# Kernel tuning notes

Hardware: AMD Instinct MI355X
Metric: run time of the kernel (lower is better)

Reference implementation:

```python
import jax, jax.numpy as jnp
import numpy as np

L = 4          # num transformer layers
C = 128        # embed_dim
P = 16         # patch size
NH = 8         # num heads
HD = C // NH   # head dim
SCALE = HD ** -0.5
THRESH = [0.001, 0.0012, 0.0015, 0.002]
EPS = 1e-5


def _ln(x, w, b):
    mu = jnp.mean(x, -1, keepdims=True)
    v = jnp.mean(jnp.square(x - mu), -1, keepdims=True)
    return (x - mu) * jax.lax.rsqrt(v + EPS) * w + b


def _attn(x, qw, qb, ow, ob):
    B, N, _ = x.shape
    qkv = (x @ qw + qb).reshape(B, N, 3, NH, HD)
    q, k, v = jnp.moveaxis(qkv, 2, 0)                      # each [B,N,NH,HD]
    q = q.transpose(0, 2, 1, 3)
    k = k.transpose(0, 2, 1, 3)
    v = v.transpose(0, 2, 1, 3)                            # [B,NH,N,HD]
    probs = jax.nn.softmax(jnp.einsum('bhnd,bhmd->bhnm', q, k) * SCALE, axis=-1)
    o = jnp.einsum('bhnm,bhmd->bhnd', probs, v).transpose(0, 2, 1, 3).reshape(B, N, C)
    return o @ ow + ob, probs


def _layer(x, i, ln1_w, ln1_b, qkv_w, qkv_b, out_w, out_b, ln2_w, ln2_b, w1, b1, w2, b2):
    a, probs = _attn(_ln(x, ln1_w[i], ln1_b[i]), qkv_w[i], qkv_b[i], out_w[i], out_b[i])
    x = x + a
    h = jax.nn.gelu(_ln(x, ln2_w[i], ln2_b[i]) @ w1[i] + b1[i], approximate=False)
    return x + h @ w2[i] + b2[i], probs


def forward(conv_w, conv_b, cls_token, pos_embed, ln1_w, ln1_b, qkv_w, qkv_b,
            out_w, out_b, ln2_w, ln2_b, mlp_w1, mlp_b1, mlp_w2, mlp_b2, x, meta=None):
    B = x.shape[0]
    Hh, Ww = x.shape[2] // P, x.shape[3] // P
    # patch embed == conv with kernel=stride=P, expressed as a patch matmul
    xr = x.reshape(B, 3, Hh, P, Ww, P).transpose(0, 2, 4, 1, 3, 5).reshape(B, Hh * Ww, 3 * P * P)
    tok = xr @ conv_w.reshape(C, -1).T + conv_b           # [B, nH*nW, C]
    x = jnp.concatenate([jnp.broadcast_to(cls_token, (B, 1, C)), tok], axis=1) + pos_embed
    meta_out = []
    for i in range(L):
        x, probs = _layer(x, i, ln1_w, ln1_b, qkv_w, qkv_b, out_w, out_b,
                          ln2_w, ln2_b, mlp_w1, mlp_b1, mlp_w2, mlp_b2)
        if i < L - 1:
            cls_t, tokens = x[:, :1], x[:, 1:]
            if meta is None:
                am = jnp.mean(probs[:, :, 1:, 0], axis=1)  # [B, N] attn of tokens to cls
                keep = am > THRESH[i]
                fb = keep.sum(1) == 0                      # fallback: keep argmax token
                keep = keep | (fb[:, None] & (jnp.arange(am.shape[1])[None, :] == jnp.argmax(am, 1)[:, None]))
                count = keep.sum(1)
                order = jnp.argsort(~keep, axis=1)         # stable: kept tokens first, in order
                mk = int(jnp.max(count))
                order, count = np.asarray(order), np.asarray(count)
                meta_out.append((order, count, mk))
            else:
                order, count, mk = meta[i]
            g = jnp.take_along_axis(tokens, jnp.asarray(order[:, :mk])[:, :, None], axis=1)
            valid = (jnp.arange(mk)[None, :] < jnp.asarray(count)[:, None]).astype(tokens.dtype)
            x = jnp.concatenate([cls_t, g * valid[:, :, None]], axis=1)
            # original re-adds pos_embed[0:1+mk] regardless of which tokens survived
            x = x + jnp.concatenate([pos_embed[:, :1], pos_embed[:, 1:1 + mk]], axis=1)
    return x, meta_out


def setup_inputs() -> dict:
    key = jax.random.key(0)
    ks = jax.random.split(key, 8)
    def w(k, shape, fan_in):
        return jax.random.normal(k, shape, jnp.float32) / np.float32(np.sqrt(fan_in))
    N_POS = (512 // P) * (512 // P) + 1  # 1025
    return {
        'conv_w': w(ks[0], (C, 3, P, P), 3 * P * P),
        'conv_b': jnp.zeros((C,), jnp.float32),
        'cls_token': jnp.zeros((1, 1, C), jnp.float32),
        'pos_embed': 0.02 * jax.random.truncated_normal(ks[1], -2.0, 2.0, (1, N_POS, C), jnp.float32),
        'ln1_w': jnp.ones((L, C), jnp.float32), 'ln1_b': jnp.zeros((L, C), jnp.float32),
        'qkv_w': w(ks[2], (L, C, 3 * C), C), 'qkv_b': jnp.zeros((L, 3 * C), jnp.float32),
        'out_w': w(ks[3], (L, C, C), C), 'out_b': jnp.zeros((L, C), jnp.float32),
        'ln2_w': jnp.ones((L, C), jnp.float32), 'ln2_b': jnp.zeros((L, C), jnp.float32),
        'mlp_w1': w(ks[4], (L, C, 4 * C), C), 'mlp_b1': jnp.zeros((L, 4 * C), jnp.float32),
        'mlp_w2': w(ks[5], (L, 4 * C, C), 4 * C), 'mlp_b2': jnp.zeros((L, C), jnp.float32),
        'x': jax.random.normal(ks[6], (8, 3, 512, 512), jnp.float32),
    }


def reference(conv_w, conv_b, cls_token, pos_embed, ln1_w, ln1_b, qkv_w, qkv_b,
              out_w, out_b, ln2_w, ln2_b, mlp_w1, mlp_b1, mlp_w2, mlp_b2, x):
    out, _ = forward(conv_w, conv_b, cls_token, pos_embed, ln1_w, ln1_b, qkv_w, qkv_b,
                     out_w, out_b, ln2_w, ln2_b, mlp_w1, mlp_b1, mlp_w2, mlp_b2, x)
    return out
```

## Files before the change

### kernel.cpp

```cpp
#include <hip/hip_runtime.h>
#include <hip/hip_bf16.h>
#include <math.h>

typedef __hip_bfloat16 bf16;
typedef __attribute__((ext_vector_type(4))) _Float16 half4;
typedef __attribute__((ext_vector_type(4))) float f32x4;

#define NMAX 1025
#define TMAX 1024
#define BATCH 8
#define CH 128
#define NHEAD 8
#define HDIM 16
#define MMAX (BATCH * NMAX)
#define QGRID 17
#define VSTRIDE 1028
#define POSZ 1049600
#define KCHUNK 192

__device__ __forceinline__ float b2f(bf16 v) { return __bfloat162float(v); }

__device__ __forceinline__ bool is_bf16(const void* ln1w_raw) {
    return ((const unsigned*)ln1w_raw)[0] == 0x3F803F80u;
}
__device__ __forceinline__ float ldsel(const void* p, size_t i, bool bf) {
    return bf ? __bfloat162float(((const bf16*)p)[i]) : ((const float*)p)[i];
}

struct CvtDesc { const void* src; float* dst; int cnt; };
struct CvtPack { CvtDesc d[15]; };

__global__ void convert_kernel(CvtPack p, const void* ln1w_raw, int* nTok) {
    bool bf = is_bf16(ln1w_raw);
    CvtDesc dd = p.d[blockIdx.y];
    int idx = blockIdx.x * 256 + threadIdx.x;
    if (idx < dd.cnt) dd.dst[idx] = ldsel(dd.src, idx, bf);
    if (blockIdx.y == 0 && idx == 0) nTok[0] = NMAX;
}

__global__ void prep_kernel(const void* conv_w, float* __restrict__ wT,
                            const void* ln1w_raw) {
    bool bf = is_bf16(ln1w_raw);
    int idx = blockIdx.x * 256 + threadIdx.x;
    if (idx < 768 * 128) {
        int k = idx >> 7, oc = idx & 127;
        wT[idx] = ldsel(conv_w, (size_t)oc * 768 + k, bf);
    }
}

__global__ __launch_bounds__(128) void patch_partial(
        const void* __restrict__ img, const float* __restrict__ wT,
        float* __restrict__ partial, const void* ln1w_raw) {
    __shared__ float pbuf[8 * KCHUNK];
    bool bf = is_bf16(ln1w_raw);
    int b = blockIdx.y;
    int g = blockIdx.x & 127;
    int kc = blockIdx.x >> 7;
    int tid = threadIdx.x;
    int t0 = g * 8;
    int kbase = kc * KCHUNK;
    const int NV = 8 * KCHUNK / 4;
    for (int i = tid; i < NV; i += 128) {
        int e = i << 2;
        int t = e / KCHUNK, kloc = e - t * KCHUNK;
        int k = kbase + kloc;
        int c = k >> 8, rem = k & 255, p1 = rem >> 4, p2 = rem & 15;
        int hw = t0 + t;
        int h = hw >> 5, w = hw & 31;
        size_t a = (((size_t)(b * 3 + c) * 512) + h * 16 + p1) * 512 + w * 16 + p2;
        float4 v;
        if (bf) {
            ushort4 u = *(const ushort4*)((const unsigned short*)img + a);
            v.x = __uint_as_float((unsigned)u.x << 16);
            v.y = __uint_as_float((unsigned)u.y << 16);
            v.z = __uint_as_float((unsigned)u.z << 16);
            v.w = __uint_as_float((unsigned)u.w << 16);
        } else {
            v = *(const float4*)((const float*)img + a);
        }
        *(float4*)&pbuf[e] = v;
    }
    __syncthreads();
    float acc[8];
#pragma unroll
    for (int t = 0; t < 8; t++) acc[t] = 0.f;
    const float* wc = wT + (size_t)kbase * 128;
    for (int k4 = 0; k4 < KCHUNK; k4 += 4) {
        float w0 = wc[(k4 + 0) * 128 + tid];
        float w1 = wc[(k4 + 1) * 128 + tid];
        float w2 = wc[(k4 + 2) * 128 + tid];
        float w3 = wc[(k4 + 3) * 128 + tid];
#pragma unroll
        for (int t = 0; t < 8; t++) {
            const float4 a = *(const float4*)&pbuf[t * KCHUNK + k4];
            acc[t] = fmaf(a.x, w0, acc[t]);
            acc[t] = fmaf(a.y, w1, acc[t]);
            acc[t] = fmaf(a.z, w2, acc[t]);
            acc[t] = fmaf(a.w, w3, acc[t]);
        }
    }
    float* pp = partial + ((size_t)(kc * 8 + b) * 1024 + t0) * 128 + tid;
#pragma unroll
    for (int t = 0; t < 8; t++) pp[(size_t)t * 128] = acc[t];
}

__global__ __launch_bounds__(256) void patch_reduce(
        const float* __restrict__ partial, const float* __restrict__ conv_b,
        const float* __restrict__ cls_tok, const float* __restrict__ pos,
        float* __restrict__ out) {
    if (blockIdx.x == 4096) {
        for (int i = threadIdx.x; i < 8 * 128; i += 256) {
            int b = i >> 7, c = i & 127;
            out[(size_t)(b * NMAX) * CH + c] = cls_tok[c] + pos[c];
        }
        return;
    }
    int idx = blockIdx.x * 256 + threadIdx.x;
    int tg = idx >> 7;
    int col = idx & 127;
    int b = tg >> 10, tok = tg & 1023;
    size_t pi = ((size_t)b * 1024 + tok) * 128 + col;
    const size_t PSTRIDE = (size_t)8 * 1024 * 128;
    float v = partial[pi] + partial[pi + PSTRIDE]
            + partial[pi + 2 * PSTRIDE] + partial[pi + 3 * PSTRIDE];
    out[((size_t)(b * NMAX) + 1 + tok) * CH + col] =
        v + conv_b[col] + pos[(size_t)(1 + tok) * CH + col];
}

template <int K, int NCOL, int CTILE, int ROWS, bool LN, bool GELU_ACT,
          bool RESID, bool QKV_SPLIT>
__global__ void mm_kernel(const float* __restrict__ A, const float* __restrict__ W,
                          const float* __restrict__ bias, const float* __restrict__ lnw,
                          const float* __restrict__ lnb, const float* __restrict__ R,
                          float* __restrict__ out, _Float16* __restrict__ kout,
                          _Float16* __restrict__ vout, const int* __restrict__ nPtr) {
    __shared__ float As[ROWS * K];
    int N = nPtr[0];
    int M = BATCH * N;
    int row0 = blockIdx.x * ROWS;
    if (row0 >= M) return;
    int tid = threadIdx.x;
    for (int i = tid; i < ROWS * K / 4; i += CTILE) {
        int e = i << 2;
        int r = e / K, rem = e % K;
        float4 v;
        int row = row0 + r;
        if (row < M)
            v = *(const float4*)&A[(size_t)row * K + rem];
        else
            v = make_float4(0.f, 0.f, 0.f, 0.f);
        *(float4*)&As[r * K + rem] = v;
    }
    __syncthreads();
    if (LN) {
        int wid = tid >> 6, lane = tid & 63;
        const int NW = CTILE / 64;
        float wl0 = lnw[lane], wl1 = lnw[64 + lane];
        float bl0 = lnb[lane], bl1 = lnb[64 + lane];
        for (int r = wid; r < ROWS; r += NW) {
            float x0 = As[r * K + lane], x1 = As[r * K + 64 + lane];
            float s = x0 + x1;
#pragma unroll
            for (int off = 32; off; off >>= 1) s += __shfl_xor(s, off);
            float mu = s * (1.f / 128.f);
            float d0 = x0 - mu, d1 = x1 - mu;
            float v = d0 * d0 + d1 * d1;
#pragma unroll
            for (int off = 32; off; off >>= 1) v += __shfl_xor(v, off);
            float inv = 1.f / sqrtf(v * (1.f / 128.f) + 1e-5f);
            As[r * K + lane] = d0 * inv * wl0 + bl0;
            As[r * K + 64 + lane] = d1 * inv * wl1 + bl1;
        }
        __syncthreads();
    }
    float acc[ROWS];
#pragma unroll
    for (int r = 0; r < ROWS; r++) acc[r] = 0.f;
    int col = tid;
    for (int k4 = 0; k4 < K; k4 += 4) {
        float w0 = W[(size_t)(k4 + 0) * NCOL + col];
        float w1 = W[(size_t)(k4 + 1) * NCOL + col];
        float w2 = W[(size_t)(k4 + 2) * NCOL + col];
        float w3 = W[(size_t)(k4 + 3) * NCOL + col];
#pragma unroll
        for (int r = 0; r < ROWS; r++) {
            const float4 a = *(const float4*)&As[r * K + k4];
            acc[r] = fmaf(a.x, w0, acc[r]);
            acc[r] = fmaf(a.y, w1, acc[r]);
            acc[r] = fmaf(a.z, w2, acc[r]);
            acc[r] = fmaf(a.w, w3, acc[r]);
        }
    }
    float bv = bias[col];
    int rmax = min(ROWS, M - row0);
    if (QKV_SPLIT) {
        int part = col >> 7;
        int c128 = col & 127;
        int hh = c128 >> 4, dd = c128 & 15;
        for (int r = 0; r < rmax; r++) {
            float v = acc[r] + bv;
            int row = row0 + r;
            if (part == 0) {
                out[(size_t)row * 128 + c128] = v;
            } else {
                int bb = row / N, nn = row - (row / N) * N;
                if (part == 1) {
                    _Float16 hi = (_Float16)v;
                    _Float16 lo = (_Float16)(v - (float)hi);
                    size_t kb2 = ((size_t)(bb * 8 + hh) * NMAX + nn) * 32 + dd;
                    kout[kb2] = hi;
                    kout[kb2 + 16] = lo;
                } else {
                    vout[((size_t)(bb * 8 + hh) * 16 + dd) * VSTRIDE + nn] = (_Float16)v;
                }
            }
        }
        if (blockIdx.x == 0 && part == 2) {
            int zn = min(16, VSTRIDE - N);
            for (int bb = 0; bb < 8; bb++) {
                size_t rb = ((size_t)((bb * 8 + hh) * 16 + dd)) * VSTRIDE;
                for (int i = 0; i < zn; i++) vout[rb + N + i] = (_Float16)0.f;
            }
            if (hh == 7 && dd == 15) {
                for (int i = 0; i < 16; i++)
                    vout[(size_t)1024 * VSTRIDE + i] = (_Float16)0.f;
            }
        }
    } else {
        for (int r = 0; r < rmax; r++) {
            float v = acc[r] + bv;
            if (GELU_ACT) v = 0.5f * v * (1.f + erff(v * 0.70710678118654752f));
            if (RESID) v += R[(size_t)(row0 + r) * NCOL + col];
            out[(size_t)(row0 + r) * NCOL + col] = v;
        }
    }
}

__global__ __launch_bounds__(256) void attn_kernel(
        const float* __restrict__ qbuf, const _Float16* __restrict__ kbuf,
        const _Float16* __restrict__ vbuf, float* __restrict__ oout,
        float* __restrict__ clsp, const int* __restrict__ nPtr) {
    int N = nPtr[0];
    int bid = blockIdx.x;
    int b = bid & 7;
    int h = (bid >> 3) & 7;
    int qg = bid >> 6;
    int wave = threadIdx.x >> 6;
    int lane = threadIdx.x & 63;
    int qt = qg * 4 + wave;
    if (qt * 16 >= N) return;
    int ql = lane & 15;
    int hig = lane >> 4;
    int nq = qt * 16 + ql;
    int nqc = min(nq, N - 1);
    half4 qhi, qlo;
    {
        const float4 qv = *(const float4*)(qbuf + ((size_t)(b * N + nqc)) * 128 + h * HDIM + hig * 4);
        float q0 = qv.x * 0.25f, q1 = qv.y * 0.25f, q2 = qv.z * 0.25f, q3 = qv.w * 0.25f;
        qhi[0] = (_Float16)q0; qlo[0] = (_Float16)(q0 - (float)qhi[0]);
        qhi[1] = (_Float16)q1; qlo[1] = (_Float16)(q1 - (float)qhi[1]);
        qhi[2] = (_Float16)q2; qlo[2] = (_Float16)(q2 - (float)qhi[2]);
        qhi[3] = (_Float16)q3; qlo[3] = (_Float16)(q3 - (float)qhi[3]);
    }
    const _Float16* kb = kbuf + (size_t)(b * 8 + h) * NMAX * 32;
    const _Float16* vt = vbuf + ((size_t)(b * 8 + h) * 16 + ql) * VSTRIDE;
    f32x4 of = {0.f, 0.f, 0.f, 0.f};
    const f32x4 zz = {0.f, 0.f, 0.f, 0.f};
    float m = -3.0e38f, l = 0.f, s0raw = 0.f;
    int ntFull = N >> 4;
    int t = 0;
    for (; t + 2 <= ntFull; t += 2) {
        int k0 = t * 16;
        const _Float16* kpA = kb + ((size_t)(k0 + ql)) * 32 + hig * 4;
        const _Float16* kpB = kpA + 16 * 32;
        half4 khiA = *(const half4*)(kpA);
        half4 kloA = *(const half4*)(kpA + 16);
        half4 khiB = *(const half4*)(kpB);
        half4 kloB = *(const half4*)(kpB + 16);
        f32x4 sA1 = __builtin_amdgcn_mfma_f32_16x16x16f16(khiA, qhi, zz, 0, 0, 0);
        f32x4 sB1 = __builtin_amdgcn_mfma_f32_16x16x16f16(khiB, qhi, zz, 0, 0, 0);
        f32x4 sA2 = __builtin_amdgcn_mfma_f32_16x16x16f16(khiA, qlo, zz, 0, 0, 0);
        f32x4 sB2 = __builtin_amdgcn_mfma_f32_16x16x16f16(khiB, qlo, zz, 0, 0, 0);
        sA2 = __builtin_amdgcn_mfma_f32_16x16x16f16(kloA, qhi, sA2, 0, 0, 0);
        sB2 = __builtin_amdgcn_mfma_f32_16x16x16f16(kloB, qhi, sB2, 0, 0, 0);
        f32x4 saA = sA1 + sA2;
        f32x4 saB = sB1 + sB2;
        if (t == 0) s0raw = saA[0];
        float mcA = fmaxf(fmaxf(saA[0], saA[1]), fmaxf(saA[2], saA[3]));
        float mcB = fmaxf(fmaxf(saB[0], saB[1]), fmaxf(saB[2], saB[3]));
        float mc = fmaxf(mcA, mcB);
        mc = fmaxf(mc, __shfl_xor(mc, 16));
        mc = fmaxf(mc, __shfl_xor(mc, 32));
        if (!__all(mc <= m)) {
            float mnew = fmaxf(m, mc);
            float corr = __expf(m - mnew);
            l *= corr;
#pragma unroll
            for (int r = 0; r < 4; r++)
                of[r] *= __shfl(corr, hig * 4 + r);
            m = mnew;
        }
        float pA0 = __expf(saA[0] - m), pA1 = __expf(saA[1] - m);
        float pA2 = __expf(saA[2] - m), pA3 = __expf(saA[3] - m);
        float pB0 = __expf(saB[0] - m), pB1 = __expf(saB[1] - m);
        float pB2 = __expf(saB[2] - m), pB3 = __expf(saB[3] - m);
        l += ((pA0 + pA1) + (pA2 + pA3)) + ((pB0 + pB1) + (pB2 + pB3));
        half4 pfA, pfB;
        pfA[0] = (_Float16)pA0; pfA[1] = (_Float16)pA1;
        pfA[2] = (_Float16)pA2; pfA[3] = (_Float16)pA3;
        pfB[0] = (_Float16)pB0; pfB[1] = (_Float16)pB1;
        pfB[2] = (_Float16)pB2; pfB[3] = (_Float16)pB3;
        half4 vfA = *(const half4*)(vt + k0 + hig * 4);
        half4 vfB = *(const half4*)(vt + k0 + 16 + hig * 4);
        of = __builtin_amdgcn_mfma_f32_16x16x16f16(pfA, vfA, of, 0, 0, 0);
        of = __builtin_amdgcn_mfma_f32_16x16x16f16(pfB, vfB, of, 0, 0, 0);
    }
    if (t < ntFull) {
        int k0 = t * 16;
        const _Float16* kp = kb + ((size_t)(k0 + ql)) * 32 + hig * 4;
        half4 khi = *(const half4*)(kp);
        half4 klo = *(const half4*)(kp + 16);
        f32x4 s1 = __builtin_amdgcn_mfma_f32_16x16x16f16(khi, qhi, zz, 0, 0, 0);
        f32x4 s2 = __builtin_amdgcn_mfma_f32_16x16x16f16(khi, qlo, zz, 0, 0, 0);
        s2 = __builtin_amdgcn_mfma_f32_16x16x16f16(klo, qhi, s2, 0, 0, 0);
        f32x4 sa = s1 + s2;
        if (t == 0) s0raw = sa[0];
        float mc = fmaxf(fmaxf(sa[0], sa[1]), fmaxf(sa[2], sa[3]));
        mc = fmaxf(mc, __shfl_xor(mc, 16));
        mc = fmaxf(mc, __shfl_xor(mc, 32));
        if (!__all(mc <= m)) {
            float mnew = fmaxf(m, mc);
            float corr = __expf(m - mnew);
            l *= corr;
#pragma unroll
            for (int r = 0; r < 4; r++)
                of[r] *= __shfl(corr, hig * 4 + r);
            m = mnew;
        }
        float p0 = __expf(sa[0] - m), p1 = __expf(sa[1] - m);
        float p2 = __expf(sa[2] - m), p3 = __expf(sa[3] - m);
        l += (p0 + p1) + (p2 + p3);
        half4 pf;
        pf[0] = (_Float16)p0; pf[1] = (_Float16)p1;
        pf[2] = (_Float16)p2; pf[3] = (_Float16)p3;
        half4 vf = *(const half4*)(vt + k0 + hig * 4);
        of = __builtin_amdgcn_mfma_f32_16x16x16f16(pf, vf, of, 0, 0, 0);
        t++;
    }
    int k0t = ntFull * 16;
    if (k0t < N) {
        int kk = min(k0t + ql, N - 1);
        const _Float16* kp = kb + (size_t)kk * 32 + hig * 4;
        half4 khi = *(const half4*)(kp);
        half4 klo = *(const half4*)(kp + 16);
        f32x4 s1 = __builtin_amdgcn_mfma_f32_16x16x16f16(khi, qhi, zz, 0, 0, 0);
        f32x4 s2 = __builtin_amdgcn_mfma_f32_16x16x16f16(khi, qlo, zz, 0, 0, 0);
        s2 = __builtin_amdgcn_mfma_f32_16x16x16f16(klo, qhi, s2, 0, 0, 0);
        f32x4 sa = s1 + s2;
        if (ntFull == 0) s0raw = sa[0];
        float s0 = (k0t + hig * 4 + 0 < N) ? sa[0] : -3.0e38f;
        float s1m = (k0t + hig * 4 + 1 < N) ? sa[1] : -3.0e38f;
        float s2m = (k0t + hig * 4 + 2 < N) ? sa[2] : -3.0e38f;
        float s3m = (k0t + hig * 4 + 3 < N) ? sa[3] : -3.0e38f;
        float mc = fmaxf(fmaxf(s0, s1m), fmaxf(s2m, s3m));
        mc = fmaxf(mc, __shfl_xor(mc, 16));
        mc = fmaxf(mc, __shfl_xor(mc, 32));
        if (!__all(mc <= m)) {
            float mnew = fmaxf(m, mc);
            float corr = __expf(m - mnew);
            l *= corr;
#pragma unroll
            for (int r = 0; r < 4; r++)
                of[r] *= __shfl(corr, hig * 4 + r);
            m = mnew;
        }
        float p0 = __expf(s0 - m);
        float p1 = __expf(s1m - m);
        float p2 = __expf(s2m - m);
        float p3 = __expf(s3m - m);
        l += (p0 + p1) + (p2 + p3);
        half4 pf;
        pf[0] = (_Float16)p0; pf[1] = (_Float16)p1;
        pf[2] = (_Float16)p2; pf[3] = (_Float16)p3;
        half4 vf = *(const half4*)(vt + k0t + hig * 4);
        of = __builtin_amdgcn_mfma_f32_16x16x16f16(pf, vf, of, 0, 0, 0);
    }
    l += __shfl_xor(l, 16);
    l += __shfl_xor(l, 32);
    float linv = 1.f / l;
#pragma unroll
    for (int r = 0; r < 4; r++) {
        int qq = qt * 16 + hig * 4 + r;
        if (qq < N) {
            float ov = of[r] * __shfl(linv, hig * 4 + r);
            oout[((size_t)(b * N + qq)) * 128 + h * HDIM + ql] = ov;
        }
    }
    if (hig == 0 && nq >= 1 && nq < N) {
        clsp[(size_t)(b * 8 + h) * TMAX + (nq - 1)] = __expf(s0raw - m) * linv;
    }
}

__global__ __launch_bounds__(1024) void prune_kernel(const float* __restrict__ clsp,
                                                     int* __restrict__ order,
                                                     int* __restrict__ cnt,
                                                     const int* __restrict__ nPtr, int layer) {
    __shared__ int sdata[1024];
    __shared__ float wv_[16];
    __shared__ int wi_[16];
    __shared__ int wc_[16];
    __shared__ int sArg, sCnt0;
    int b = blockIdx.x;
    int t = threadIdx.x;
    int N = nPtr[0];
    int T = N - 1;
    float am = -1.f;
    if (t < T) {
        float s = 0.f;
#pragma unroll
        for (int h = 0; h < 8; h++) s += clsp[((size_t)(b * 8 + h)) * TMAX + t];
        am = s * 0.125f;
    }
    const double TH[4] = {0.001, 0.0012, 0.0015, 0.002};
    int keep = (t < T) && ((double)am > TH[layer]);
    float bv = am;
    int bi = t;
    int kc = keep;
#pragma unroll
    for (int off = 32; off; off >>= 1) {
        float ov = __shfl_xor(bv, off);
        int oi = __shfl_xor(bi, off);
        if (ov > bv || (ov == bv && oi < bi)) { bv = ov; bi = oi; }
        kc += __shfl_xor(kc, off);
    }
    int wid = t >> 6, lane = t & 63;
    if (lane == 0) { wv_[wid] = bv; wi_[wid] = bi; wc_[wid] = kc; }
    __syncthreads();
    if (t == 0) {
        float Bv = wv_[0];
        int Bi = wi_[0], C = 0;
        for (int w = 0; w < 16; w++) {
            C += wc_[w];
            if (wv_[w] > Bv || (wv_[w] == Bv && wi_[w] < Bi)) { Bv = wv_[w]; Bi = wi_[w]; }
        }
        sArg = Bi;
        sCnt0 = C;
    }
    __syncthreads();
    if (sCnt0 == 0) keep = (t == sArg) && (t < T);
    sdata[t] = keep;
    __syncthreads();
    for (int off = 1; off < 1024; off <<= 1) {
        int v = sdata[t];
        int add = (t >= off) ? sdata[t - off] : 0;
        __syncthreads();
        sdata[t] = v + add;
        __syncthreads();
    }
    int incl = sdata[t];
    int total = sdata[1023];
    if (t < T) {
        if (keep)
            order[b * TMAX + (incl - 1)] = t;
        else
            order[b * TMAX + total + t - incl] = t;
    }
    if (t == 0) cnt[b] = total;
}

__global__ __launch_bounds__(256) void gather_kernel(
        const float* __restrict__ xin, float* __restrict__ xout,
        const int* __restrict__ order, const int* __restrict__ cnt,
        const float* __restrict__ pos, const int* __restrict__ nPtr,
        int* __restrict__ nNext) {
    int Nold = nPtr[0];
    int mk = cnt[0];
#pragma unroll
    for (int i = 1; i < 8; i++) mk = max(mk, cnt[i]);
    int Nnew = mk + 1;
    if (blockIdx.x == 0 && blockIdx.y == 0 && threadIdx.x == 0) nNext[0] = Nnew;
    int b = blockIdx.y;
    int j = blockIdx.x * 2 + (threadIdx.x >> 7);
    int c = threadIdx.x & 127;
    if (j >= Nnew) return;
    float v;
    if (j == 0)
        v = xin[((size_t)(b * Nold)) * CH + c];
    else {
        int src = order[b * TMAX + (j - 1)];
        v = (j - 1 < cnt[b]) ? xin[((size_t)(b * Nold + 1 + src)) * CH + c] : 0.f;
    }
    xout[((size_t)(b * Nnew + j)) * CH + c] = v + pos[(size_t)j * CH + c];
}

__global__ void outconv_kernel(const float* __restrict__ xin, void* __restrict__ out,
                               int total, const void* ln1w_raw) {
    bool bf = is_bf16(ln1w_raw);
    int i = blockIdx.x * 256 + threadIdx.x;
    if (i < total) {
        if (bf) ((bf16*)out)[i] = __float2bfloat16(xin[i]);
        else    ((float*)out)[i] = xin[i];
    }
}

extern "C" void kernel_launch(void* const* d_in, const int* in_sizes, int n_in,
                              void* d_out, int out_size, void* d_ws, size_t ws_size,
                              hipStream_t stream) {
    const void* conv_w = d_in[0];
    const void* conv_b = d_in[1];
    const void* cls_token = d_in[2];
    const void* pos_embed = d_in[3];
    const void* ln1_w = d_in[4];
    const void* ln1_b = d_in[5];
    const void* qkv_w = d_in[6];
    const void* qkv_b = d_in[7];
    const void* out_w = d_in[8];
    const void* out_b = d_in[9];
    const void* ln2_w = d_in[10];
    const void* ln2_b = d_in[11];
    const void* mlp_w1 = d_in[12];
    const void* mlp_b1 = d_in[13];
    const void* mlp_w2 = d_in[14];
    const void* mlp_b2 = d_in[15];
    const void* img = d_in[16];

    float* ws = (float*)d_ws;
    size_t off = 0;
    float* bufA = ws + off; off += POSZ;
    float* bufB = ws + off; off += POSZ;
    float* obuf = ws + off; off += POSZ;
    float* tmp  = ws + off; off += (size_t)BATCH * NMAX * 512;
    float* wT   = ws + off; off += 768 * 128;
    float* clsp = ws + off; off += (size_t)BATCH * NHEAD * TMAX;
    int* order  = (int*)(ws + off); off += BATCH * TMAX;
    int* cnt    = (int*)(ws + off); off += 16;
    int* nTok   = (int*)(ws + off); off += 16;
    float* wts  = ws + off;
    const size_t wts_total = 924544;

    float* qbuf = tmp;
    _Float16* kbuf = (_Float16*)(tmp + POSZ);
    _Float16* vbuf = (_Float16*)(tmp + 2 * POSZ);

    float* f_conv_b = wts + 0;
    float* f_cls    = wts + 128;
    float* f_pos    = wts + 256;
    float* f_ln1w   = wts + 131456;
    float* f_ln1b   = wts + 131968;
    float* f_qkvw   = wts + 132480;
    float* f_qkvb   = wts + 329088;
    float* f_outw   = wts + 330624;
    float* f_outb   = wts + 396160;
    float* f_ln2w   = wts + 396672;
    float* f_ln2b   = wts + 397184;
    float* f_w1     = wts + 397696;
    float* f_b1     = wts + 659840;
    float* f_w2     = wts + 661888;
    float* f_b2     = wts + 924032;

    CvtPack pk;
    pk.d[0]  = {conv_b,    f_conv_b, 128};
    pk.d[1]  = {cls_token, f_cls,    128};
    pk.d[2]  = {pos_embed, f_pos,    131200};
    pk.d[3]  = {ln1_w,     f_ln1w,   512};
    pk.d[4]  = {ln1_b,     f_ln1b,   512};
    pk.d[5]  = {qkv_w,     f_qkvw,   196608};
    pk.d[6]  = {qkv_b,     f_qkvb,   1536};
    pk.d[7]  = {out_w,     f_outw,   65536};
    pk.d[8]  = {out_b,     f_outb,   512};
    pk.d[9]  = {ln2_w,     f_ln2w,   512};
    pk.d[10] = {ln2_b,     f_ln2b,   512};
    pk.d[11] = {mlp_w1,    f_w1,     262144};
    pk.d[12] = {mlp_b1,    f_b1,     2048};
    pk.d[13] = {mlp_w2,    f_w2,     262144};
    pk.d[14] = {mlp_b2,    f_b2,     512};

    convert_kernel<<<dim3(1024, 15), 256, 0, stream>>>(pk, ln1_w, nTok);
    prep_kernel<<<(768 * 128 + 255) / 256, 256, 0, stream>>>(conv_w, wT, ln1_w);
    patch_partial<<<dim3(512, BATCH), 128, 0, stream>>>(img, wT, tmp, ln1_w);
    patch_reduce<<<4097, 256, 0, stream>>>(tmp, f_conv_b, f_cls, f_pos, bufA);

    float* xc = bufA;
    float* xalt = bufB;
    const int GR8 = (MMAX + 7) / 8;

    for (int i = 0; i < 4; i++) {
        const int* nP = nTok + i;
        mm_kernel<128, 384, 384, 8, true, false, false, true>
            <<<GR8, 384, 0, stream>>>(
            xc, f_qkvw + (size_t)i * 128 * 384, f_qkvb + i * 384,
            f_ln1w + i * 128, f_ln1b + i * 128, nullptr, qbuf, kbuf, vbuf, nP);
        attn_kernel<<<QGRID * 64, 256, 0, stream>>>(
            qbuf, kbuf, vbuf, qbuf, clsp, nP);
        mm_kernel<128, 128, 128, 8, false, false, true, false>
            <<<GR8, 128, 0, stream>>>(
            qbuf, f_outw + (size_t)i * 128 * 128, f_outb + i * 128,
            nullptr, nullptr, xc, xalt, nullptr, nullptr, nP);
        mm_kernel<128, 512, 512, 8, true, true, false, false>
            <<<GR8, 512, 0, stream>>>(
            xalt, f_w1 + (size_t)i * 128 * 512, f_b1 + i * 512,
            f_ln2w + i * 128, f_ln2b + i * 128, nullptr, tmp, nullptr, nullptr, nP);
        mm_kernel<512, 128, 128, 8, false, false, true, false>
            <<<GR8, 128, 0, stream>>>(
            tmp, f_w2 + (size_t)i * 512 * 128, f_b2 + i * 128,
            nullptr, nullptr, xalt, xc, nullptr, nullptr, nP);
        if (i < 3) {
            prune_kernel<<<BATCH, 1024, 0, stream>>>(clsp, order, cnt, nP, i);
            gather_kernel<<<dim3((NMAX + 1) / 2, BATCH), 256, 0, stream>>>(
                xc, xalt, order, cnt, f_pos, nP, nTok + i + 1);
            float* t2 = xc; xc = xalt; xalt = t2;
        }
    }
    outconv_kernel<<<(out_size + 255) / 256, 256, 0, stream>>>(xc, d_out, out_size, ln1_w);
}
```

Before: 634.1 us.

## Split patch embed across two thread teams, lazy softmax rescale, smaller row tiles

patch_partial now runs 256 threads per block, with two teams of 128 each computing 4 tokens instead of one team computing 8. This halves per-thread accumulator work and adds parallelism. The attention online softmax skips the cross-lane max reduction and rescale unless a local score exceeds the running max by more than 8, which trades fewer shuffles and branches for slightly larger exponent ranges. The out-projection and MLP-down matmuls use 4-row tiles with twice as many blocks.

```diff
diff --git a/kernel.cpp b/kernel.cpp
--- a/kernel.cpp
+++ b/kernel.cpp
@@ -48,7 +48,7 @@
     }
 }
 
-__global__ __launch_bounds__(128) void patch_partial(
+__global__ __launch_bounds__(256) void patch_partial(
         const void* __restrict__ img, const float* __restrict__ wT,
         float* __restrict__ partial, const void* ln1w_raw) {
     __shared__ float pbuf[8 * KCHUNK];
@@ -60,7 +60,7 @@
     int t0 = g * 8;
     int kbase = kc * KCHUNK;
     const int NV = 8 * KCHUNK / 4;
-    for (int i = tid; i < NV; i += 128) {
+    for (int i = tid; i < NV; i += 256) {
         int e = i << 2;
         int t = e / KCHUNK, kloc = e - t * KCHUNK;
         int k = kbase + kloc;
@@ -81,27 +81,30 @@
         *(float4*)&pbuf[e] = v;
     }
     __syncthreads();
-    float acc[8];
-#pragma unroll
-    for (int t = 0; t < 8; t++) acc[t] = 0.f;
+    int team = tid >> 7;
+    int col = tid & 127;
+    float acc[4];
+#pragma unroll
+    for (int t = 0; t < 4; t++) acc[t] = 0.f;
     const float* wc = wT + (size_t)kbase * 128;
+    const float* pb = pbuf + team * 4 * KCHUNK;
     for (int k4 = 0; k4 < KCHUNK; k4 += 4) {
-        float w0 = wc[(k4 + 0) * 128 + tid];
-        float w1 = wc[(k4 + 1) * 128 + tid];
-        float w2 = wc[(k4 + 2) * 128 + tid];
-        float w3 = wc[(k4 + 3) * 128 + tid];
-#pragma unroll
-        for (int t = 0; t < 8; t++) {
-            const float4 a = *(const float4*)&pbuf[t * KCHUNK + k4];
+        float w0 = wc[(k4 + 0) * 128 + col];
+        float w1 = wc[(k4 + 1) * 128 + col];
+        float w2 = wc[(k4 + 2) * 128 + col];
+        float w3 = wc[(k4 + 3) * 128 + col];
+#pragma unroll
+        for (int t = 0; t < 4; t++) {
+            const float4 a = *(const float4*)&pb[t * KCHUNK + k4];
             acc[t] = fmaf(a.x, w0, acc[t]);
             acc[t] = fmaf(a.y, w1, acc[t]);
             acc[t] = fmaf(a.z, w2, acc[t]);
             acc[t] = fmaf(a.w, w3, acc[t]);
         }
     }
-    float* pp = partial + ((size_t)(kc * 8 + b) * 1024 + t0) * 128 + tid;
-#pragma unroll
-    for (int t = 0; t < 8; t++) pp[(size_t)t * 128] = acc[t];
+    float* pp = partial + ((size_t)(kc * 8 + b) * 1024 + t0 + team * 4) * 128 + col;
+#pragma unroll
+    for (int t = 0; t < 4; t++) pp[(size_t)t * 128] = acc[t];
 }
 
 __global__ __launch_bounds__(256) void patch_reduce(
@@ -288,10 +291,10 @@
         if (t == 0) s0raw = saA[0];
         float mcA = fmaxf(fmaxf(saA[0], saA[1]), fmaxf(saA[2], saA[3]));
         float mcB = fmaxf(fmaxf(saB[0], saB[1]), fmaxf(saB[2], saB[3]));
-        float mc = fmaxf(mcA, mcB);
-        mc = fmaxf(mc, __shfl_xor(mc, 16));
-        mc = fmaxf(mc, __shfl_xor(mc, 32));
-        if (!__all(mc <= m)) {
+        float mloc = fmaxf(mcA, mcB);
+        if (!__all(mloc <= m + 8.f)) {
+            float mc = fmaxf(mloc, __shfl_xor(mloc, 16));
+            mc = fmaxf(mc, __shfl_xor(mc, 32));
             float mnew = fmaxf(m, mc);
             float corr = __expf(m - mnew);
             l *= corr;
@@ -325,10 +328,10 @@
         s2 = __builtin_amdgcn_mfma_f32_16x16x16f16(klo, qhi, s2, 0, 0, 0);
         f32x4 sa = s1 + s2;
         if (t == 0) s0raw = sa[0];
-        float mc = fmaxf(fmaxf(sa[0], sa[1]), fmaxf(sa[2], sa[3]));
-        mc = fmaxf(mc, __shfl_xor(mc, 16));
-        mc = fmaxf(mc, __shfl_xor(mc, 32));
-        if (!__all(mc <= m)) {
+        float mloc = fmaxf(fmaxf(sa[0], sa[1]), fmaxf(sa[2], sa[3]));
+        if (!__all(mloc <= m + 8.f)) {
+            float mc = fmaxf(mloc, __shfl_xor(mloc, 16));
+            mc = fmaxf(mc, __shfl_xor(mc, 32));
             float mnew = fmaxf(m, mc);
             float corr = __expf(m - mnew);
             l *= corr;
@@ -362,10 +365,10 @@
         float s1m = (k0t + hig * 4 + 1 < N) ? sa[1] : -3.0e38f;
         float s2m = (k0t + hig * 4 + 2 < N) ? sa[2] : -3.0e38f;
         float s3m = (k0t + hig * 4 + 3 < N) ? sa[3] : -3.0e38f;
-        float mc = fmaxf(fmaxf(s0, s1m), fmaxf(s2m, s3m));
-        mc = fmaxf(mc, __shfl_xor(mc, 16));
-        mc = fmaxf(mc, __shfl_xor(mc, 32));
-        if (!__all(mc <= m)) {
+        float mloc = fmaxf(fmaxf(s0, s1m), fmaxf(s2m, s3m));
+        if (!__all(mloc <= m + 8.f)) {
+            float mc = fmaxf(mloc, __shfl_xor(mloc, 16));
+            mc = fmaxf(mc, __shfl_xor(mc, 32));
             float mnew = fmaxf(m, mc);
             float corr = __expf(m - mnew);
             l *= corr;
@@ -577,12 +580,13 @@
 
     convert_kernel<<<dim3(1024, 15), 256, 0, stream>>>(pk, ln1_w, nTok);
     prep_kernel<<<(768 * 128 + 255) / 256, 256, 0, stream>>>(conv_w, wT, ln1_w);
-    patch_partial<<<dim3(512, BATCH), 128, 0, stream>>>(img, wT, tmp, ln1_w);
+    patch_partial<<<dim3(512, BATCH), 256, 0, stream>>>(img, wT, tmp, ln1_w);
     patch_reduce<<<4097, 256, 0, stream>>>(tmp, f_conv_b, f_cls, f_pos, bufA);
 
     float* xc = bufA;
     float* xalt = bufB;
     const int GR8 = (MMAX + 7) / 8;
+    const int GR4 = (MMAX + 3) / 4;
 
     for (int i = 0; i < 4; i++) {
         const int* nP = nTok + i;
@@ -592,16 +596,16 @@
             f_ln1w + i * 128, f_ln1b + i * 128, nullptr, qbuf, kbuf, vbuf, nP);
         attn_kernel<<<QGRID * 64, 256, 0, stream>>>(
             qbuf, kbuf, vbuf, qbuf, clsp, nP);
-        mm_kernel<128, 128, 128, 8, false, false, true, false>
-            <<<GR8, 128, 0, stream>>>(
+        mm_kernel<128, 128, 128, 4, false, false, true, false>
+            <<<GR4, 128, 0, stream>>>(
             qbuf, f_outw + (size_t)i * 128 * 128, f_outb + i * 128,
             nullptr, nullptr, xc, xalt, nullptr, nullptr, nP);
         mm_kernel<128, 512, 512, 8, true, true, false, false>
             <<<GR8, 512, 0, stream>>>(
             xalt, f_w1 + (size_t)i * 128 * 512, f_b1 + i * 512,
             f_ln2w + i * 128, f_ln2b + i * 128, nullptr, tmp, nullptr, nullptr, nP);
-        mm_kernel<512, 128, 128, 8, false, false, true, false>
-            <<<GR8, 128, 0, stream>>>(
+        mm_kernel<512, 128, 128, 4, false, false, true, false>
+            <<<GR4, 128, 0, stream>>>(
             tmp, f_w2 + (size_t)i * 512 * 128, f_b2 + i * 128,
             nullptr, nullptr, xalt, xc, nullptr, nullptr, nP);
         if (i < 3) {
```

Measured after the change: 779.9 us. 23.0% more time.
